# Optimization experiments

Hardware: AMD Instinct MI355X
Metric: run time of the kernel (lower is better)

Reference implementation:

```python
import jax, jax.numpy as jnp
import numpy as np

H = 3584        # hidden_size
NH = 16         # num_attention_heads
HD = 256        # head_dim
NKV = 8         # num_key_value_heads
GROUPS = NH // NKV
B, S = 2, 2048
SOFTCAP = 50.0
SCALE = 256.0 ** -0.5   # query_pre_attn_scalar ** -0.5
ROPE_BASE = 10000.0
NEG = -1e9


def _rotate_half(x):
    x1, x2 = jnp.split(x, 2, axis=-1)
    return jnp.concatenate([-x2, x1], axis=-1)


def _apply_rope(x, cos, sin):
    # x: [b, h, s, d]; cos/sin: [s, d]
    return x * cos[None, None] + _rotate_half(x) * sin[None, None]


def setup_inputs() -> dict:
    key = jax.random.key(0)
    k1, k2, k3, k4, k5 = jax.random.split(key, 5)
    hidden_states = jax.random.normal(k1, (B, S, H), dtype=jnp.float32)
    # additive causal mask [1, 1, S, S]
    causal = jnp.tril(jnp.ones((S, S), dtype=bool))
    attention_mask = jnp.where(causal, 0.0, NEG).astype(jnp.float32)[None, None]
    Wq = jax.random.normal(k2, (H, NH * HD), dtype=jnp.float32) * 0.02
    Wk = jax.random.normal(k3, (H, NKV * HD), dtype=jnp.float32) * 0.02
    Wv = jax.random.normal(k4, (H, NKV * HD), dtype=jnp.float32) * 0.02
    Wo = jax.random.normal(k5, (NH * HD, H), dtype=jnp.float32) * 0.02
    return {"hidden_states": hidden_states, "attention_mask": attention_mask,
            "Wq": Wq, "Wk": Wk, "Wv": Wv, "Wo": Wo}


def reference(hidden_states, attention_mask, Wq, Wk, Wv, Wo):
    b, s, _ = hidden_states.shape
    q = (hidden_states @ Wq).reshape(b, s, NH, HD).transpose(0, 2, 1, 3)   # [b,nh,s,d]
    k = (hidden_states @ Wk).reshape(b, s, NKV, HD).transpose(0, 2, 1, 3)  # [b,nkv,s,d]
    v = (hidden_states @ Wv).reshape(b, s, NKV, HD).transpose(0, 2, 1, 3)

    # RoPE (HF-style: freqs duplicated, rotate_half)
    pos = jnp.arange(s, dtype=jnp.float32)
    inv_freq = 1.0 / (ROPE_BASE ** (jnp.arange(0, HD, 2, dtype=jnp.float32) / HD))
    freqs = pos[:, None] * inv_freq[None, :]          # [s, d/2]
    emb = jnp.concatenate([freqs, freqs], axis=-1)    # [s, d]
    cos, sin = jnp.cos(emb), jnp.sin(emb)
    q = _apply_rope(q, cos, sin)
    k = _apply_rope(k, cos, sin)

    # repeat_kv for GQA
    k = jnp.repeat(k, GROUPS, axis=1)  # [b,nh,s,d]
    v = jnp.repeat(v, GROUPS, axis=1)

    scores = jnp.einsum('bhsd,bhtd->bhst', q, k) * SCALE
    # tanh logit softcapping
    scores = jnp.tanh(scores / SOFTCAP) * SOFTCAP
    scores = scores + attention_mask
    probs = jax.nn.softmax(scores.astype(jnp.float32), axis=-1).astype(q.dtype)
    out = jnp.einsum('bhst,bhtd->bhsd', probs, v)
    out = out.transpose(0, 2, 1, 3).reshape(b, s, NH * HD)
    return out @ Wo
```

## Files before the change

### kernel.cpp

```cpp
#include <hip/hip_runtime.h>
#include <cstdint>
#include <cstddef>

typedef __bf16 bf16x8 __attribute__((ext_vector_type(8)));
typedef float  f32x4  __attribute__((ext_vector_type(4)));
typedef unsigned short u16;

#define GLDS16(GP, LP) __builtin_amdgcn_global_load_lds( \
    (const __attribute__((address_space(1))) void*)(GP), \
    (__attribute__((address_space(3))) void*)(LP), 16, 0, 0)

__device__ __forceinline__ float b2f(u16 u) {
  unsigned int x = ((unsigned int)u) << 16;
  return __builtin_bit_cast(float, x);
}
__device__ __forceinline__ u16 f2b(float f) {
  unsigned int u = __builtin_bit_cast(unsigned int, f);
  unsigned int r = (u + 0x7fffu + ((u >> 16) & 1u)) >> 16;
  return (u16)r;
}

constexpr int Bc  = 2;
constexpr int Sc  = 2048;
constexpr int Hc  = 3584;
constexpr int NHc = 16;
constexpr int HDc = 256;
constexpr int NKV = 8;
constexpr int QD  = NHc * HDc;
constexpr int QS  = 8192;
constexpr float SCALE   = 0.0625f;
constexpr float CAP     = 50.0f;
constexpr float INV_CAP = 1.0f / 50.0f;

__device__ __forceinline__ float softcap(float raw) {
  float y = raw * (SCALE * INV_CAP);
  float a = __builtin_fabsf(y);
  float e = __expf(-2.0f * a);
  float t = (1.0f - e) * __builtin_amdgcn_rcpf(1.0f + e);
  return copysignf(t, y) * CAP;
}

__global__ void rope_table_k(float* __restrict__ cosT, float* __restrict__ sinT) {
  int idx = blockIdx.x * 256 + threadIdx.x;
  int s = idx >> 7, i = idx & 127;
  float inv = expf((float)i * -0.0719557841560639f);
  float ang = (float)s * inv;
  cosT[idx] = cosf(ang);
  sinT[idx] = sinf(ang);
}

__global__ void cvt_f32_bf16(const float4* __restrict__ in, ushort4* __restrict__ out, int n4) {
  int i = blockIdx.x * 256 + threadIdx.x;
  int st = gridDim.x * 256;
  for (; i < n4; i += st) {
    float4 v = in[i];
    ushort4 u;
    u.x = f2b(v.x); u.y = f2b(v.y); u.z = f2b(v.z); u.w = f2b(v.w);
    out[i] = u;
  }
}

__global__ void transpose_cvt(const float* __restrict__ in, u16* __restrict__ out, int R, int C) {
  __shared__ float t[32][33];
  int c0 = blockIdx.x * 32, r0 = blockIdx.y * 32;
  int tx = threadIdx.x, ty = threadIdx.y;
#pragma unroll
  for (int i = 0; i < 4; i++)
    t[ty + i * 8][tx] = in[(size_t)(r0 + ty + i * 8) * C + c0 + tx];
  __syncthreads();
#pragma unroll
  for (int i = 0; i < 4; i++)
    out[(size_t)(c0 + ty + i * 8) * R + r0 + tx] = f2b(t[tx][ty + i * 8]);
}

__global__ void transpose_v(const u16* __restrict__ QKV, u16* __restrict__ Vt) {
  __shared__ u16 t[32][33];
  int b = blockIdx.z >> 3, kvh = blockIdx.z & 7;
  int s0 = blockIdx.x * 32, d0 = blockIdx.y * 32;
  int tx = threadIdx.x, ty = threadIdx.y;
#pragma unroll
  for (int i = 0; i < 4; i++)
    t[ty + i * 8][tx] = QKV[(size_t)(b * Sc + s0 + ty + i * 8) * QS + 6144 + kvh * HDc + d0 + tx];
  __syncthreads();
#pragma unroll
  for (int i = 0; i < 4; i++)
    Vt[(size_t)((b * NKV + kvh) * HDc + d0 + ty + i * 8) * Sc + s0 + tx] = t[tx][ty + i * 8];
}

template <int NH>
__global__ void rope_apply(u16* __restrict__ X, const float* __restrict__ cosT,
                           const float* __restrict__ sinT) {
  constexpr int LS = (NH == 16) ? 4 : 3;
  int idx = blockIdx.x * 256 + threadIdx.x;
  const int i4 = (idx & 31) << 2;
  const int h = (idx >> 5) & (NH - 1);
  const int row = idx >> (5 + LS);
  const int s = row & (Sc - 1);
  u16* p = X + (size_t)row * QS + h * 256 + i4;
  ushort4 lo = *(const ushort4*)p;
  ushort4 hi = *(const ushort4*)(p + 128);
  float4 c = *(const float4*)(cosT + s * 128 + i4);
  float4 sn = *(const float4*)(sinT + s * 128 + i4);
  ushort4 nlo, nhi;
  { float xl = b2f(lo.x), xh = b2f(hi.x);
    nlo.x = f2b(xl * c.x - xh * sn.x); nhi.x = f2b(xh * c.x + xl * sn.x); }
  { float xl = b2f(lo.y), xh = b2f(hi.y);
    nlo.y = f2b(xl * c.y - xh * sn.y); nhi.y = f2b(xh * c.y + xl * sn.y); }
  { float xl = b2f(lo.z), xh = b2f(hi.z);
    nlo.z = f2b(xl * c.z - xh * sn.z); nhi.z = f2b(xh * c.z + xl * sn.z); }
  { float xl = b2f(lo.w), xh = b2f(hi.w);
    nlo.w = f2b(xl * c.w - xh * sn.w); nhi.w = f2b(xh * c.w + xl * sn.w); }
  *(ushort4*)p = nlo;
  *(ushort4*)(p + 128) = nhi;
}

template <typename OT>
__global__ __launch_bounds__(512, 1) void gemm256(const u16* __restrict__ A,
                                                  const u16* __restrict__ Bt,
                                                  OT* __restrict__ C,
                                                  int M, int N, int K, int GM) {
  __shared__ alignas(16) u16 As[2][256 * 64];
  __shared__ alignas(16) u16 Bs[2][256 * 64];
  const int nwg = gridDim.x;
  const int cpx = nwg >> 3;
  const int wgid = (blockIdx.x & 7) * cpx + (blockIdx.x >> 3);
  const int m0 = (wgid % GM) * 256;
  const int n0 = (wgid / GM) * 256;
  const int tid = threadIdx.x;
  const int lane = tid & 63;
  const int w = tid >> 6;
  const int wm = w >> 2, wn = w & 3;
  const int lg = lane >> 4, lr = lane & 15;
  const int nkt = K >> 6;

  auto STAGE = [&](int buf, int kt) {
    const int k0 = kt * 64;
#pragma unroll
    for (int i = 0; i < 4; i++) {
      int c = i * 512 + tid;
      int row = c >> 3, slot = c & 7;
      GLDS16(A + (size_t)(m0 + row) * K + k0 + (slot ^ (row & 7)) * 8,
             (char*)As[buf] + c * 16);
    }
#pragma unroll
    for (int i = 0; i < 4; i++) {
      int c = i * 512 + tid;
      int row = c >> 3, slot = c & 7;
      GLDS16(Bt + (size_t)(n0 + row) * K + k0 + (slot ^ (row & 7)) * 8,
             (char*)Bs[buf] + c * 16);
    }
  };

  f32x4 acc[8][4] = {};

  STAGE(0, 0);
  STAGE(1, 1);
  asm volatile("s_waitcnt vmcnt(8)" ::: "memory");
  __builtin_amdgcn_sched_barrier(0);
  __builtin_amdgcn_s_barrier();

  for (int kt = 0; kt < nkt; ++kt) {
    const int buf = kt & 1;
#pragma unroll
    for (int q = 0; q < 4; ++q) {
      const int qm = q >> 1, qn = q & 1;
      bf16x8 af[4][2], bfr[2][2];
#pragma unroll
      for (int i = 0; i < 4; i++)
#pragma unroll
        for (int ks = 0; ks < 2; ks++) {
          int row = wm * 128 + qm * 64 + i * 16 + lr;
          int sl = (ks * 4 + lg) ^ (row & 7);
          af[i][ks] = *(const bf16x8*)&As[buf][row * 64 + sl * 8];
        }
#pragma unroll
      for (int j = 0; j < 2; j++)
#pragma unroll
        for (int ks = 0; ks < 2; ks++) {
          int row = wn * 64 + qn * 32 + j * 16 + lr;
          int sl = (ks * 4 + lg) ^ (row & 7);
          bfr[j][ks] = *(const bf16x8*)&Bs[buf][row * 64 + sl * 8];
        }
      asm volatile("s_waitcnt lgkmcnt(0)" ::: "memory");
      __builtin_amdgcn_sched_barrier(0);
      if (q == 3) {
        __builtin_amdgcn_s_barrier();
        if (kt + 2 < nkt) STAGE(buf, kt + 2);
      }
      __builtin_amdgcn_s_setprio(1);
#pragma unroll
      for (int i = 0; i < 4; i++)
#pragma unroll
        for (int j = 0; j < 2; j++)
#pragma unroll
          for (int ks = 0; ks < 2; ks++)
            acc[qm * 4 + i][qn * 2 + j] = __builtin_amdgcn_mfma_f32_16x16x32_bf16(
                af[i][ks], bfr[j][ks], acc[qm * 4 + i][qn * 2 + j], 0, 0, 0);
      __builtin_amdgcn_s_setprio(0);
    }
    if (kt + 1 < nkt) {
      if (kt + 2 < nkt)
        asm volatile("s_waitcnt vmcnt(8)" ::: "memory");
      else
        asm volatile("s_waitcnt vmcnt(0)" ::: "memory");
      __builtin_amdgcn_sched_barrier(0);
      __builtin_amdgcn_s_barrier();
    }
  }

#pragma unroll
  for (int i = 0; i < 8; i++) {
    const int row = m0 + wm * 128 + i * 16 + lg * 4;
#pragma unroll
    for (int j = 0; j < 4; j++) {
      const int col = n0 + wn * 64 + j * 16 + lr;
#pragma unroll
      for (int r = 0; r < 4; r++) {
        if constexpr (sizeof(OT) == 2)
          C[(size_t)(row + r) * N + col] = f2b(acc[i][j][r]);
        else
          C[(size_t)(row + r) * N + col] = acc[i][j][r];
      }
    }
  }
}

__global__ __launch_bounds__(512, 1) void attn_fwd(const u16* __restrict__ QKV,
                                                   const u16* __restrict__ Vt,
                                                   u16* __restrict__ AO) {
  constexpr int KVB = 64;
  __shared__ alignas(16) u16 Ks[2][KVB * 256];
  __shared__ alignas(16) u16 Vs[2][256 * KVB];
  __shared__ alignas(16) u16 Ps[8][16][72];
  const int bx = blockIdx.x, h = blockIdx.y, b = blockIdx.z;
  const int qt = b ? (15 - bx) : bx;
  const int q0 = qt * 128;
  const int kvh = h >> 1;
  const int tid = threadIdx.x, w = tid >> 6, lane = tid & 63;
  const int lg = lane >> 4, lr = lane & 15;

  bf16x8 qf[8];
  {
    const u16* qp = QKV + (size_t)(b * Sc + q0 + w * 16 + lr) * QS + h * HDc + lg * 8;
#pragma unroll
    for (int kk = 0; kk < 8; kk++) qf[kk] = *(const bf16x8*)(qp + kk * 32);
  }

  f32x4 o[16] = {};
  float m_r[4], l_r[4];
#pragma unroll
  for (int r = 0; r < 4; r++) { m_r[r] = -1e30f; l_r[r] = 0.0f; }
  const int my_qrow = q0 + w * 16 + lg * 4;
  const int wave_min_row = q0 + w * 16;
  const int wave_max_row = q0 + w * 16 + 15;

  const u16* kbase = QKV + (size_t)(b * Sc) * QS + 4096 + kvh * HDc;
  const u16* vbase = Vt + (size_t)((b * NKV + kvh) * HDc) * Sc;

  auto STAGE = [&](int buf, int t0) {
#pragma unroll
    for (int i = 0; i < 4; i++) {
      int c = i * 512 + tid;
      int row = c >> 5, slot = c & 31;
      int gs = slot ^ (row & 7);
      GLDS16(kbase + (size_t)(t0 + row) * QS + gs * 8, (char*)Ks[buf] + c * 16);
    }
#pragma unroll
    for (int i = 0; i < 4; i++) {
      int c = i * 512 + tid;
      int d = c >> 3, slot = c & 7;
      int gs = slot ^ (d & 7);
      GLDS16(vbase + (size_t)d * Sc + t0 + gs * 8, (char*)Vs[buf] + c * 16);
    }
  };

  const int nt = 2 * qt + 2;
  int cur = 0;
  STAGE(0, 0);
  for (int ti = 0; ti < nt; ++ti) {
    const int t0 = ti * 64;
    if (ti + 1 < nt) {
      STAGE(cur ^ 1, t0 + 64);
      asm volatile("s_waitcnt vmcnt(8)" ::: "memory");
    } else {
      asm volatile("s_waitcnt vmcnt(0)" ::: "memory");
    }
    __builtin_amdgcn_sched_barrier(0);
    __builtin_amdgcn_s_barrier();

    if (t0 <= wave_max_row) {
      const u16* KsT = Ks[cur];
      const u16* VsT = Vs[cur];

      f32x4 sc[4];
#pragma unroll
      for (int j = 0; j < 4; j++) {
        f32x4 a = {0.f, 0.f, 0.f, 0.f};
        const int row = j * 16 + lr;
#pragma unroll
        for (int kk = 0; kk < 8; kk++) {
          int s0 = (kk * 4 + lg) ^ (lr & 7);
          bf16x8 kf = *(const bf16x8*)&KsT[row * 256 + s0 * 8];
          a = __builtin_amdgcn_mfma_f32_16x16x32_bf16(qf[kk], kf, a, 0, 0, 0);
        }
        sc[j] = a;
      }

      float tmax[4] = {-1e30f, -1e30f, -1e30f, -1e30f};
      if (t0 + 63 > wave_min_row) {
#pragma unroll
        for (int j = 0; j < 4; j++)
#pragma unroll
          for (int r = 0; r < 4; r++) {
            float x = softcap(sc[j][r]);
            if (t0 + j * 16 + lr > my_qrow + r) x = -1e9f;
            sc[j][r] = x;
            tmax[r] = fmaxf(tmax[r], x);
          }
      } else {
#pragma unroll
        for (int j = 0; j < 4; j++)
#pragma unroll
          for (int r = 0; r < 4; r++) {
            float x = softcap(sc[j][r]);
            sc[j][r] = x;
            tmax[r] = fmaxf(tmax[r], x);
          }
      }
#pragma unroll
      for (int xm = 1; xm < 16; xm <<= 1)
#pragma unroll
        for (int r = 0; r < 4; r++) tmax[r] = fmaxf(tmax[r], __shfl_xor(tmax[r], xm, 64));

      bool need = false;
#pragma unroll
      for (int r = 0; r < 4; r++) need |= (tmax[r] > m_r[r] + 8.0f);
      if (__any(need)) {
        float scal[4];
#pragma unroll
        for (int r = 0; r < 4; r++) {
          float mn = fmaxf(m_r[r], tmax[r]);
          scal[r] = __expf(m_r[r] - mn);
          m_r[r] = mn;
          l_r[r] *= scal[r];
        }
#pragma unroll
        for (int df = 0; df < 16; df++)
#pragma unroll
          for (int r = 0; r < 4; r++) o[df][r] *= scal[r];
      }

      float psum[4] = {0.f, 0.f, 0.f, 0.f};
#pragma unroll
      for (int j = 0; j < 4; j++)
#pragma unroll
        for (int r = 0; r < 4; r++) {
          float p = __expf(sc[j][r] - m_r[r]);
          psum[r] += p;
          Ps[w][lg * 4 + r][j * 16 + lr] = f2b(p);
        }
#pragma unroll
      for (int xm = 1; xm < 16; xm <<= 1)
#pragma unroll
        for (int r = 0; r < 4; r++) psum[r] += __shfl_xor(psum[r], xm, 64);
#pragma unroll
      for (int r = 0; r < 4; r++) l_r[r] += psum[r];

      bf16x8 pf0 = *(const bf16x8*)&Ps[w][lr][lg * 8];
      bf16x8 pf1 = *(const bf16x8*)&Ps[w][lr][32 + lg * 8];
#pragma unroll
      for (int df = 0; df < 16; df++) {
        const int d = df * 16 + lr;
        int s0 = lg ^ (lr & 7);
        int s1 = (4 + lg) ^ (lr & 7);
        bf16x8 vf0 = *(const bf16x8*)&VsT[d * KVB + s0 * 8];
        o[df] = __builtin_amdgcn_mfma_f32_16x16x32_bf16(pf0, vf0, o[df], 0, 0, 0);
        bf16x8 vf1 = *(const bf16x8*)&VsT[d * KVB + s1 * 8];
        o[df] = __builtin_amdgcn_mfma_f32_16x16x32_bf16(pf1, vf1, o[df], 0, 0, 0);
      }
    }

    __builtin_amdgcn_s_barrier();
    cur ^= 1;
  }

  float inv_l[4];
#pragma unroll
  for (int r = 0; r < 4; r++) inv_l[r] = 1.0f / l_r[r];
  u16* op = AO + (size_t)(b * Sc + my_qrow) * QD + h * HDc + lr;
#pragma unroll
  for (int df = 0; df < 16; df++)
#pragma unroll
    for (int r = 0; r < 4; r++)
      op[(size_t)r * QD + df * 16] = f2b(o[df][r] * inv_l[r]);
}

extern "C" void kernel_launch(void* const* d_in, const int* in_sizes, int n_in,
                              void* d_out, int out_size, void* d_ws, size_t ws_size,
                              hipStream_t stream) {
  (void)in_sizes; (void)n_in; (void)out_size; (void)ws_size;
  const float* hs = (const float*)d_in[0];
  const float* Wq = (const float*)d_in[2];
  const float* Wk = (const float*)d_in[3];
  const float* Wv = (const float*)d_in[4];
  const float* Wo = (const float*)d_in[5];
  float* out = (float*)d_out;
  char* ws = (char*)d_ws;

  float* cosT = (float*)(ws + 0);
  float* sinT = (float*)(ws + 1048576);
  u16* hsb    = (u16*)(ws + 2097152);
  u16* Wqkvt  = (u16*)(ws + 31457280);
  u16* Wot    = (u16*)(ws + 90177536);
  u16* QKVb   = (u16*)(ws + 119537664);
  u16* Vtr    = hsb;
  u16* AO     = Wqkvt;

  dim3 tb32x8(32, 8);

  rope_table_k<<<1024, 256, 0, stream>>>(cosT, sinT);
  cvt_f32_bf16<<<2048, 256, 0, stream>>>((const float4*)hs, (ushort4*)hsb, (Bc * Sc * Hc) / 4);
  transpose_cvt<<<dim3(QD / 32, Hc / 32), tb32x8, 0, stream>>>(Wq, Wqkvt, Hc, QD);
  transpose_cvt<<<dim3(2048 / 32, Hc / 32), tb32x8, 0, stream>>>(Wk, Wqkvt + (size_t)4096 * Hc, Hc, 2048);
  transpose_cvt<<<dim3(2048 / 32, Hc / 32), tb32x8, 0, stream>>>(Wv, Wqkvt + (size_t)6144 * Hc, Hc, 2048);
  transpose_cvt<<<dim3(Hc / 32, QD / 32), tb32x8, 0, stream>>>(Wo, Wot, QD, Hc);

  gemm256<u16><<<dim3(16 * 32), 512, 0, stream>>>(hsb, Wqkvt, QKVb, Bc * Sc, QS, Hc, 16);

  rope_apply<16><<<8192, 256, 0, stream>>>(QKVb, cosT, sinT);
  rope_apply<8><<<4096, 256, 0, stream>>>(QKVb + 4096, cosT, sinT);
  transpose_v<<<dim3(Sc / 32, HDc / 32, Bc * NKV), tb32x8, 0, stream>>>(QKVb, Vtr);

  attn_fwd<<<dim3(16, NHc, Bc), 512, 0, stream>>>(QKVb, Vtr, AO);

  gemm256<float><<<dim3(16 * 14), 512, 0, stream>>>(AO, Wot, out, Bc * Sc, Hc, QD, 16);
}
```

Baseline: 676.5 us.

## Regroup GEMM tile order and halve B-fragment LDS reloads per k-step

```diff
diff --git a/kernel.cpp b/kernel.cpp
--- a/kernel.cpp
+++ b/kernel.cpp
@@ -124,8 +124,12 @@
   const int nwg = gridDim.x;
   const int cpx = nwg >> 3;
   const int wgid = (blockIdx.x & 7) * cpx + (blockIdx.x >> 3);
-  const int m0 = (wgid % GM) * 256;
-  const int n0 = (wgid / GM) * 256;
+  const int GN = nwg / GM;
+  const int width = 8 * GN;
+  const int grp = wgid / width;
+  const int rem = wgid - grp * width;
+  const int m0 = (grp * 8 + (rem & 7)) * 256;
+  const int n0 = (rem >> 3) * 256;
   const int tid = threadIdx.x;
   const int lane = tid & 63;
   const int w = tid >> 6;
@@ -161,43 +165,57 @@
 
   for (int kt = 0; kt < nkt; ++kt) {
     const int buf = kt & 1;
-#pragma unroll
-    for (int q = 0; q < 4; ++q) {
-      const int qm = q >> 1, qn = q & 1;
-      bf16x8 af[4][2], bfr[2][2];
-#pragma unroll
-      for (int i = 0; i < 4; i++)
-#pragma unroll
-        for (int ks = 0; ks < 2; ks++) {
-          int row = wm * 128 + qm * 64 + i * 16 + lr;
-          int sl = (ks * 4 + lg) ^ (row & 7);
-          af[i][ks] = *(const bf16x8*)&As[buf][row * 64 + sl * 8];
-        }
-#pragma unroll
-      for (int j = 0; j < 2; j++)
-#pragma unroll
-        for (int ks = 0; ks < 2; ks++) {
-          int row = wn * 64 + qn * 32 + j * 16 + lr;
-          int sl = (ks * 4 + lg) ^ (row & 7);
-          bfr[j][ks] = *(const bf16x8*)&Bs[buf][row * 64 + sl * 8];
-        }
-      asm volatile("s_waitcnt lgkmcnt(0)" ::: "memory");
-      __builtin_amdgcn_sched_barrier(0);
-      if (q == 3) {
-        __builtin_amdgcn_s_barrier();
-        if (kt + 2 < nkt) STAGE(buf, kt + 2);
-      }
-      __builtin_amdgcn_s_setprio(1);
-#pragma unroll
-      for (int i = 0; i < 4; i++)
-#pragma unroll
-        for (int j = 0; j < 2; j++)
-#pragma unroll
-          for (int ks = 0; ks < 2; ks++)
-            acc[qm * 4 + i][qn * 2 + j] = __builtin_amdgcn_mfma_f32_16x16x32_bf16(
-                af[i][ks], bfr[j][ks], acc[qm * 4 + i][qn * 2 + j], 0, 0, 0);
-      __builtin_amdgcn_s_setprio(0);
-    }
+    bf16x8 bfr[4][2], af[4][2];
+#pragma unroll
+    for (int j = 0; j < 4; j++)
+#pragma unroll
+      for (int ks = 0; ks < 2; ks++) {
+        int row = wn * 64 + j * 16 + lr;
+        int sl = (ks * 4 + lg) ^ (row & 7);
+        bfr[j][ks] = *(const bf16x8*)&Bs[buf][row * 64 + sl * 8];
+      }
+#pragma unroll
+    for (int i = 0; i < 4; i++)
+#pragma unroll
+      for (int ks = 0; ks < 2; ks++) {
+        int row = wm * 128 + i * 16 + lr;
+        int sl = (ks * 4 + lg) ^ (row & 7);
+        af[i][ks] = *(const bf16x8*)&As[buf][row * 64 + sl * 8];
+      }
+    asm volatile("s_waitcnt lgkmcnt(0)" ::: "memory");
+    __builtin_amdgcn_sched_barrier(0);
+    __builtin_amdgcn_s_setprio(1);
+#pragma unroll
+    for (int i = 0; i < 4; i++)
+#pragma unroll
+      for (int j = 0; j < 4; j++)
+#pragma unroll
+        for (int ks = 0; ks < 2; ks++)
+          acc[i][j] = __builtin_amdgcn_mfma_f32_16x16x32_bf16(
+              af[i][ks], bfr[j][ks], acc[i][j], 0, 0, 0);
+    __builtin_amdgcn_s_setprio(0);
+#pragma unroll
+    for (int i = 0; i < 4; i++)
+#pragma unroll
+      for (int ks = 0; ks < 2; ks++) {
+        int row = wm * 128 + 64 + i * 16 + lr;
+        int sl = (ks * 4 + lg) ^ (row & 7);
+        af[i][ks] = *(const bf16x8*)&As[buf][row * 64 + sl * 8];
+      }
+    asm volatile("s_waitcnt lgkmcnt(0)" ::: "memory");
+    __builtin_amdgcn_sched_barrier(0);
+    __builtin_amdgcn_s_barrier();
+    if (kt + 2 < nkt) STAGE(buf, kt + 2);
+    __builtin_amdgcn_s_setprio(1);
+#pragma unroll
+    for (int i = 0; i < 4; i++)
+#pragma unroll
+      for (int j = 0; j < 4; j++)
+#pragma unroll
+        for (int ks = 0; ks < 2; ks++)
+          acc[4 + i][j] = __builtin_amdgcn_mfma_f32_16x16x32_bf16(
+              af[i][ks], bfr[j][ks], acc[4 + i][j], 0, 0, 0);
+    __builtin_amdgcn_s_setprio(0);
     if (kt + 1 < nkt) {
       if (kt + 2 < nkt)
         asm volatile("s_waitcnt vmcnt(8)" ::: "memory");
```

Measured after the change: 620.3 us. 8.3% less time.
